# Kernel tuning notes

Hardware: AMD Instinct MI355X
Metric: run time of the kernel (lower is better)

## Reference

```python
import jax, jax.numpy as jnp
import numpy as np

DS = 8        # downsample_dim
PRUNE = 0.9


def _prune(w, rate):
    # DNW-style magnitude pruning: keep top (1-rate) fraction of |w|.
    thr = jnp.percentile(jnp.abs(w), rate * 100.0)
    mask = (jnp.abs(w) >= thr).astype(w.dtype)
    # straight-through: forward uses w*mask, backward passes dense grad to w
    return w - jax.lax.stop_gradient(w - w * mask)


def _conv2d(x, k):
    return jax.lax.conv_general_dilated(
        x, k, (1, 1), 'SAME', dimension_numbers=('NCHW', 'OIHW', 'NCHW'))


def _instance_norm(x, gamma, beta, eps=1e-5):
    mu = x.mean(axis=(2, 3), keepdims=True)
    var = ((x - mu) ** 2).mean(axis=(2, 3), keepdims=True)
    xn = (x - mu) * jax.lax.rsqrt(var + eps)
    return xn * gamma[None, :, None, None] + beta[None, :, None, None]


def _graph(x, w1, w2):
    B, C, H, W = x.shape
    f = H // DS
    # average-pool down to DS x DS, flatten channels*spatial into graph nodes
    pooled = x.reshape(B, C, DS, f, DS, f).mean(axis=(3, 5))  # [B, C, DS, DS]
    nodes = pooled.reshape(B, C * DS * DS)                    # [B, N]
    h = jax.nn.relu(nodes @ _prune(w1, PRUNE).T)              # [B, feature_dim]
    out = h @ _prune(w2, PRUNE).T                             # [B, N]
    out = out.reshape(B, C, DS, DS)
    # nearest-neighbor upsample back to H x W
    out = jnp.repeat(jnp.repeat(out, f, axis=2), f, axis=3)
    return out


def setup_inputs() -> dict:
    key = jax.random.key(0)
    ks = jax.random.split(key, 4)
    B, C, H, W = 32, 256, 32, 32
    N = C * DS * DS   # 16384 nodes
    FEAT = 2048       # feature_dim
    x = jax.random.normal(ks[0], (B, C, H, W), jnp.float32)
    conv_w = jax.random.normal(ks[1], (C, C, 3, 3), jnp.float32) / np.sqrt(C * 9)
    w1 = jax.random.normal(ks[2], (FEAT, N), jnp.float32) / np.sqrt(N)
    w2 = jax.random.normal(ks[3], (N, FEAT), jnp.float32) / np.sqrt(FEAT)
    gamma = jnp.ones((C,), jnp.float32)
    beta = jnp.zeros((C,), jnp.float32)
    return {"x": x, "conv_w": conv_w, "w1": w1, "w2": w2,
            "gamma": gamma, "beta": beta, "t": 0}


def reference(x, conv_w, w1, w2, gamma, beta, t):
    # t is the ODE time; unused by the forward math (as in the original module)
    out = jax.nn.relu(x)
    out = _conv2d(out, conv_w)
    out = _graph(out, w1, w2)
    out = _instance_norm(out, gamma, beta)
    return out
```

## Files before the change

kernel.cpp:

```cpp
#include <hip/hip_runtime.h>
#include <stdint.h>


typedef float f32x4 __attribute__((ext_vector_type(4)));
typedef __bf16 bf16x8 __attribute__((ext_vector_type(8)));

#define NBATCH 32
#define NCH    256
#define NNODE  16384
#define FEATD  2048
#define KCONV  2304

static constexpr long long NW    = 33554432LL;
static constexpr double    POS_D = 0.9 * (double)(NW - 1);
static constexpr int       K0    = (int)POS_D;

static constexpr int WAVE_CAP = 768;
static constexpr int NSEG     = 4096;
static constexpr int OVCAP    = 65536;
static constexpr int EBUF_CAP = 8192;

static constexpr size_t OFF_APOOL = 0;
static constexpr size_t OFF_NODES = 9437184;
static constexpr size_t OFF_HF32  = 10485760;
static constexpr size_t OFF_HB    = 10747904;
static constexpr size_t OFF_G     = 10878976;
static constexpr size_t OFF_SHIST = 12976128;
static constexpr size_t OFF_GHIST = 12992512;
static constexpr size_t OFF_CTRL  = 13025280;
static constexpr size_t OFF_EBUF  = 13025408;
static constexpr size_t OFF_CNT   = 13058176;
static constexpr size_t OFF_BLW   = 13074560;
static constexpr size_t OFF_CBUF  = 13090944;
static constexpr size_t OFF_OVF   = OFF_CBUF + (size_t)NSEG * WAVE_CAP * 4;
static constexpr size_t WS_MIN    = OFF_OVF + (size_t)OVCAP * 4;

struct Ctrl {
  unsigned vlo, vhi, shift, nov;
  unsigned e_lo, e_hi, base_e, nex;
  unsigned b0, b1, dbg, pad;
  float thr, a, b;
  unsigned pad2;
};

__device__ __forceinline__ float prune1(float v, float thr) {
  return fabsf(v) >= thr ? v : 0.0f;
}


__global__ void k_sample_hist(const float* __restrict__ w, unsigned* __restrict__ hist) {
  __shared__ unsigned lh[4096];
  int t = threadIdx.x;
  for (int i = t; i < 4096; i += 256) lh[i] = 0;
  __syncthreads();
  const float4* p = (const float4*)(w + (size_t)blockIdx.x * 65536);
  float4 v = p[t];
  {
    unsigned k;
    k = (__float_as_uint(v.x) & 0x7fffffffu) >> 19; atomicAdd(&lh[k], 1u);
    k = (__float_as_uint(v.y) & 0x7fffffffu) >> 19; atomicAdd(&lh[k], 1u);
    k = (__float_as_uint(v.z) & 0x7fffffffu) >> 19; atomicAdd(&lh[k], 1u);
    k = (__float_as_uint(v.w) & 0x7fffffffu) >> 19; atomicAdd(&lh[k], 1u);
  }
  __syncthreads();
  for (int i = t; i < 4096; i += 256)
    if (lh[i]) atomicAdd(&hist[i], lh[i]);
}

__global__ void k_range2(const unsigned* __restrict__ hist, Ctrl* __restrict__ c) {
  __shared__ unsigned csum[256];
  __shared__ unsigned pre[256];
  __shared__ unsigned res[2];
  int t = threadIdx.x;
  unsigned loc[16];
  unsigned s = 0;
  for (int i = 0; i < 16; ++i) { loc[i] = hist[t * 16 + i]; s += loc[i]; }
  csum[t] = s;
  __syncthreads();
  if (t == 0) {
    unsigned acc = 0;
    for (int i = 0; i < 256; ++i) { pre[i] = acc; acc += csum[i]; }
  }
  __syncthreads();
  const int m = 524288, qm = 471859, MR = 2000;
  int targ[2] = { qm - MR, qm + MR };
  for (int k = 0; k < 2; ++k) {
    int r = targ[k];
    if (r < 0) r = 0;
    if (r >= m) r = m - 1;
    if ((int)pre[t] <= r && r < (int)(pre[t] + csum[t])) {
      unsigned acc = pre[t];
      for (int i = 0; i < 16; ++i) {
        acc += loc[i];
        if ((int)acc > r) { res[k] = (unsigned)(t * 16 + i); break; }
      }
    }
  }
  __syncthreads();
  if (t == 0) {
    int lo = (int)res[0];
    int hi = (int)res[1];
    if (hi - lo + 1 > 8) hi = lo + 7;
    c->vlo = (unsigned)lo << 19;
    c->vhi = (unsigned)(hi + 1) << 19;
    unsigned span = c->vhi - c->vlo;
    unsigned sh = 0;
    while ((span >> sh) > 8192u) sh++;
    c->shift = sh;
    c->nov = 0; c->nex = 0;
    c->thr = 0.f;
  }
}

__global__ void k_compact(const float* __restrict__ w, unsigned* __restrict__ cbuf,
                          unsigned* __restrict__ ovf, unsigned* __restrict__ counts,
                          unsigned* __restrict__ belows, Ctrl* __restrict__ c) {
  __shared__ unsigned lbuf[4][WAVE_CAP];
  int t = threadIdx.x, wv = t >> 6, lane = t & 63;
  unsigned vlo = c->vlo, vhi = c->vhi;
  unsigned below = 0;
  unsigned cnt = 0;
  unsigned long long lanemask = (1ull << lane) - 1ull;
  const float4* p = (const float4*)(w + (size_t)blockIdx.x * 32768);
  for (int it = 0; it < 32; ++it) {
    float4 v = p[it * 256 + t];
    float comps[4] = { v.x, v.y, v.z, v.w };
#pragma unroll
    for (int j = 0; j < 4; ++j) {
      unsigned key = __float_as_uint(comps[j]) & 0x7fffffffu;
      below += (key < vlo) ? 1u : 0u;
      bool in = (key >= vlo) && (key < vhi);
      unsigned long long msk = __ballot(in);
      if (in) {
        unsigned slot = cnt + (unsigned)__popcll(msk & lanemask);
        if (slot < (unsigned)WAVE_CAP) lbuf[wv][slot] = key;
        else {
          unsigned ps = atomicAdd(&c->nov, 1u);
          if (ps < (unsigned)OVCAP) ovf[ps] = key;
        }
      }
      cnt += (unsigned)__popcll(msk);
    }
  }
  for (int off = 1; off < 64; off <<= 1) below += __shfl_xor(below, off);
  unsigned staged = cnt < (unsigned)WAVE_CAP ? cnt : (unsigned)WAVE_CAP;
  int s = blockIdx.x * 4 + wv;
  unsigned* dst = cbuf + (size_t)s * WAVE_CAP;
  for (unsigned i = lane; i < staged; i += 64) dst[i] = lbuf[wv][i];
  if (lane == 0) { counts[s] = staged; belows[s] = below; }
}

__global__ void k_sel_hist(const unsigned* __restrict__ cbuf, const unsigned* __restrict__ ovf,
                           const unsigned* __restrict__ counts, unsigned* __restrict__ gh,
                           const Ctrl* __restrict__ c) {
  __shared__ unsigned h[8192];
  int t = threadIdx.x;
  for (int i = t; i < 8192; i += 256) h[i] = 0;
  __syncthreads();
  unsigned vlo = c->vlo, sh = c->shift;
  for (int i = 0; i < 64; ++i) {
    int s = blockIdx.x * 64 + i;
    unsigned n = counts[s];
    const unsigned* seg = cbuf + (size_t)s * WAVE_CAP;
    for (unsigned k = t; k < n; k += 256)
      atomicAdd(&h[(seg[k] - vlo) >> sh], 1u);
  }
  if (blockIdx.x == 0) {
    unsigned nov = c->nov; if (nov > (unsigned)OVCAP) nov = OVCAP;
    for (unsigned k = t; k < nov; k += 256)
      atomicAdd(&h[(ovf[k] - vlo) >> sh], 1u);
  }
  __syncthreads();
  for (int i = t; i < 8192; i += 256)
    if (h[i]) atomicAdd(&gh[i], h[i]);
}

__global__ void k_sel_bin(const unsigned* __restrict__ gh, const unsigned* __restrict__ counts,
                          const unsigned* __restrict__ belows, Ctrl* __restrict__ c) {
  __shared__ unsigned rb[256], rc[256];
  __shared__ unsigned cs[256];
  __shared__ unsigned pre[257];
  __shared__ int bsel[2];
  __shared__ unsigned pbase[2];
  __shared__ long long tot_below, tot_nin;
  int t = threadIdx.x;
  unsigned bsum = 0, csum2 = 0;
  for (int i = 0; i < 16; ++i) { bsum += belows[t * 16 + i]; csum2 += counts[t * 16 + i]; }
  rb[t] = bsum; rc[t] = csum2;
  unsigned loc[32];
  unsigned s = 0;
  for (int i = 0; i < 32; ++i) { loc[i] = gh[t * 32 + i]; s += loc[i]; }
  cs[t] = s;
  __syncthreads();
  if (t == 0) {
    unsigned acc = 0;
    for (int i = 0; i < 256; ++i) { pre[i] = acc; acc += cs[i]; }
    pre[256] = acc;
    long long a = 0, b = 0;
    for (int i = 0; i < 256; ++i) { a += rb[i]; b += rc[i]; }
    unsigned nov = c->nov; if (nov > (unsigned)OVCAP) nov = OVCAP;
    tot_below = a; tot_nin = b + nov;
    bsel[0] = 0; bsel[1] = 0; pbase[0] = 0; pbase[1] = 0;
  }
  __syncthreads();
  long long nin = tot_nin;
  long long below = tot_below;
  for (int k = 0; k < 2; ++k) {
    long long r = (long long)(K0 + k) - below;
    if (r < 0) r = 0;
    if (r >= nin) r = nin - 1;
    if ((long long)pre[t] <= r && r < (long long)pre[t] + (long long)cs[t]) {
      unsigned acc = pre[t];
      for (int i = 0; i < 32; ++i) {
        if ((long long)(acc + loc[i]) > r) { bsel[k] = t * 32 + i; pbase[k] = acc; break; }
        acc += loc[i];
      }
    }
    __syncthreads();
  }
  if (t == 0) {
    int b0 = bsel[0], b1 = bsel[1];
    c->b0 = (unsigned)b0; c->b1 = (unsigned)b1;
    c->e_lo = c->vlo + ((unsigned)b0 << c->shift);
    c->e_hi = c->vlo + ((unsigned)(b1 + 1) << c->shift);
    c->base_e = (unsigned)(below + (long long)pbase[0]);
    c->nex = 0;
  }
}

__global__ void k_extract(const unsigned* __restrict__ cbuf, const unsigned* __restrict__ ovf,
                          const unsigned* __restrict__ counts, unsigned* __restrict__ ebuf,
                          Ctrl* __restrict__ c) {
  unsigned e_lo = c->e_lo, e_hi = c->e_hi;
  int t = threadIdx.x;
  for (int i = 0; i < 64; ++i) {
    int s = blockIdx.x * 64 + i;
    unsigned n = counts[s];
    const unsigned* seg = cbuf + (size_t)s * WAVE_CAP;
    for (unsigned k = t; k < n; k += 256) {
      unsigned key = seg[k];
      if (key >= e_lo && key < e_hi) {
        unsigned p = atomicAdd(&c->nex, 1u);
        if (p < (unsigned)EBUF_CAP) ebuf[p] = key;
      }
    }
  }
  if (blockIdx.x == 0) {
    unsigned nov = c->nov; if (nov > (unsigned)OVCAP) nov = OVCAP;
    for (unsigned k = t; k < nov; k += 256) {
      unsigned key = ovf[k];
      if (key >= e_lo && key < e_hi) {
        unsigned p = atomicAdd(&c->nex, 1u);
        if (p < (unsigned)EBUF_CAP) ebuf[p] = key;
      }
    }
  }
}

__global__ void k_final(const unsigned* __restrict__ ebuf, Ctrl* __restrict__ c,
                        double frac) {
  __shared__ unsigned keys[EBUF_CAP];
  __shared__ unsigned abits, bbits;
  int t = threadIdx.x;
  int n = (int)c->nex; if (n > EBUF_CAP) n = EBUF_CAP;
  for (int i = t; i < n; i += 256) keys[i] = ebuf[i];
  if (t == 0) { abits = 0; bbits = 0; }
  __syncthreads();
  long long r0 = (long long)K0 - (long long)c->base_e;
  long long r1 = r0 + 1;
  if (r0 < 0) r0 = 0; if (r0 > n - 1) r0 = n - 1;
  if (r1 < 0) r1 = 0; if (r1 > n - 1) r1 = n - 1;
  for (int i = t; i < n; i += 256) {
    unsigned k = keys[i];
    int cl = 0, ce = 0;
    for (int j = 0; j < n; ++j) {
      cl += (keys[j] < k) ? 1 : 0;
      ce += (keys[j] <= k) ? 1 : 0;
    }
    if ((long long)cl <= r0 && r0 < (long long)ce) abits = k;
    if ((long long)cl <= r1 && r1 < (long long)ce) bbits = k;
  }
  __syncthreads();
  if (t == 0) {
    double a = (double)__uint_as_float(abits);
    double b = (double)__uint_as_float(bbits);
    c->a = (float)a; c->b = (float)b;
    c->thr = (float)(a + frac * (b - a));
  }
}


__global__ void k_pool(const float* __restrict__ x, __bf16* __restrict__ apool) {
  __shared__ float lds[4][1024];
  __shared__ float V[4][24][32];
  int t = threadIdx.x, wv = t >> 6, lane = t & 63;
  int p = blockIdx.x * 4 + wv;
  int b = p >> 8, cch = p & 255;
  const float* xp = x + (size_t)p * 1024;
  for (int q = 0; q < 4; ++q) {
    float4 v = ((const float4*)xp)[q * 64 + lane];
    int idx = (q * 64 + lane) * 4;
    lds[wv][idx + 0] = fmaxf(v.x, 0.f);
    lds[wv][idx + 1] = fmaxf(v.y, 0.f);
    lds[wv][idx + 2] = fmaxf(v.z, 0.f);
    lds[wv][idx + 3] = fmaxf(v.w, 0.f);
  }
  __syncthreads();
  for (int e = lane; e < 768; e += 64) {
    int vi = e >> 5, ccol = e & 31;
    int i = vi / 3, dy = vi % 3;
    int r0 = 4 * i + dy - 1;
    float s = 0.f;
#pragma unroll
    for (int u = 0; u < 4; ++u) {
      int r = r0 + u;
      if (r >= 0 && r < 32) s += lds[wv][r * 32 + ccol];
    }
    V[wv][vi][ccol] = s;
  }
  __syncthreads();
  int pos = lane, i = pos >> 3, j = pos & 7;
  __bf16* ap = apool + (size_t)(b * 64 + pos) * KCONV + cch * 9;
#pragma unroll
  for (int dy = 0; dy < 3; ++dy) {
    int vi = i * 3 + dy;
#pragma unroll
    for (int dx = 0; dx < 3; ++dx) {
      int c0 = 4 * j + dx - 1;
      float s = 0.f;
#pragma unroll
      for (int v4 = 0; v4 < 4; ++v4) {
        int cc = c0 + v4;
        if (cc >= 0 && cc < 32) s += V[wv][vi][cc];
      }
      ap[dy * 3 + dx] = (__bf16)(s * 0.0625f);
    }
  }
}

__global__ void k_convgemm(const __bf16* __restrict__ apool, const float* __restrict__ cw,
                           __bf16* __restrict__ nodes) {
  int t = threadIdx.x, wv = t >> 6, l = t & 63;
  int cb = blockIdx.x & 15;
  int rg = blockIdx.x >> 4;
  int row0 = rg * 256 + wv * 64;
  int cbase = cb * 16;
  int kofs = (l >> 4) * 8;
  f32x4 acc[4] = {};
  const float* aw = cw + (size_t)(cbase + (l & 15)) * KCONV + kofs;
  for (int kk = 0; kk < KCONV; kk += 32) {
    float4 a0 = *(const float4*)(aw + kk);
    float4 a1 = *(const float4*)(aw + kk + 4);
    bf16x8 af;
    af[0] = (__bf16)a0.x; af[1] = (__bf16)a0.y; af[2] = (__bf16)a0.z; af[3] = (__bf16)a0.w;
    af[4] = (__bf16)a1.x; af[5] = (__bf16)a1.y; af[6] = (__bf16)a1.z; af[7] = (__bf16)a1.w;
#pragma unroll
    for (int rt = 0; rt < 4; ++rt) {
      const __bf16* bp = apool + (size_t)(row0 + rt * 16 + (l & 15)) * KCONV + kk + kofs;
      bf16x8 bv = *(const bf16x8*)bp;
      acc[rt] = __builtin_amdgcn_mfma_f32_16x16x32_bf16(af, bv, acc[rt], 0, 0, 0);
    }
  }
#pragma unroll
  for (int rt = 0; rt < 4; ++rt) {
    int prow = row0 + rt * 16 + (l & 15);
    int bidx = prow >> 6, pos = prow & 63;
#pragma unroll
    for (int j = 0; j < 4; ++j) {
      int cc = cbase + (l >> 4) * 4 + j;
      nodes[(size_t)bidx * NNODE + cc * 64 + pos] = (__bf16)acc[rt][j];
    }
  }
}

__global__ void k_gemm1(const float* __restrict__ w1, const __bf16* __restrict__ nodes,
                        const Ctrl* __restrict__ ctrl, float* __restrict__ hf) {
  int t = threadIdx.x, wv = t >> 6, l = t & 63;
  int fb = blockIdx.x >> 5;
  int ks = blockIdx.x & 31;
  float thr = ctrl->thr;
  int kofs = (l >> 4) * 8;
  int kk0 = ks * 512;
  const float*  awp = w1 + (size_t)(fb * 64 + wv * 16 + (l & 15)) * NNODE + kk0 + kofs;
  const __bf16* b0p = nodes + (size_t)(l & 15) * NNODE + kk0 + kofs;
  const __bf16* b1p = nodes + (size_t)((l & 15) + 16) * NNODE + kk0 + kofs;
  f32x4 acc0 = {}, acc1 = {};
#pragma unroll 4
  for (int kk = 0; kk < 512; kk += 32) {
    float4 a0 = *(const float4*)(awp + kk);
    float4 a1 = *(const float4*)(awp + kk + 4);
    bf16x8 af;
    af[0] = (__bf16)prune1(a0.x, thr); af[1] = (__bf16)prune1(a0.y, thr);
    af[2] = (__bf16)prune1(a0.z, thr); af[3] = (__bf16)prune1(a0.w, thr);
    af[4] = (__bf16)prune1(a1.x, thr); af[5] = (__bf16)prune1(a1.y, thr);
    af[6] = (__bf16)prune1(a1.z, thr); af[7] = (__bf16)prune1(a1.w, thr);
    bf16x8 bv0 = *(const bf16x8*)(b0p + kk);
    bf16x8 bv1 = *(const bf16x8*)(b1p + kk);
    acc0 = __builtin_amdgcn_mfma_f32_16x16x32_bf16(af, bv0, acc0, 0, 0, 0);
    acc1 = __builtin_amdgcn_mfma_f32_16x16x32_bf16(af, bv1, acc1, 0, 0, 0);
  }
#pragma unroll
  for (int j = 0; j < 4; ++j) {
    int f = fb * 64 + wv * 16 + (l >> 4) * 4 + j;
    atomicAdd(&hf[f * 32 + (l & 15)], acc0[j]);
    atomicAdd(&hf[f * 32 + 16 + (l & 15)], acc1[j]);
  }
}

__global__ void k_relucvt(const float* __restrict__ hf, __bf16* __restrict__ hb) {
  int idx = blockIdx.x * 256 + threadIdx.x;
  float v = fmaxf(hf[idx], 0.f);
  int f = idx >> 5, b = idx & 31;
  hb[b * FEATD + f] = (__bf16)v;
}

__global__ void k_gemm2(const float* __restrict__ w2, const __bf16* __restrict__ hb,
                        const Ctrl* __restrict__ ctrl, float* __restrict__ g) {
  int t = threadIdx.x, wv = t >> 6, l = t & 63;
  int nb = blockIdx.x >> 2;
  int ks = blockIdx.x & 3;
  float thr = ctrl->thr;
  int kofs = (l >> 4) * 8;
  int kk0 = ks * 512;
  const float*  awp = w2 + (size_t)(nb * 64 + wv * 16 + (l & 15)) * FEATD + kk0 + kofs;
  const __bf16* b0p = hb + (size_t)(l & 15) * FEATD + kk0 + kofs;
  const __bf16* b1p = hb + (size_t)((l & 15) + 16) * FEATD + kk0 + kofs;
  f32x4 acc0 = {}, acc1 = {};
#pragma unroll 4
  for (int kk = 0; kk < 512; kk += 32) {
    float4 a0 = *(const float4*)(awp + kk);
    float4 a1 = *(const float4*)(awp + kk + 4);
    bf16x8 af;
    af[0] = (__bf16)prune1(a0.x, thr); af[1] = (__bf16)prune1(a0.y, thr);
    af[2] = (__bf16)prune1(a0.z, thr); af[3] = (__bf16)prune1(a0.w, thr);
    af[4] = (__bf16)prune1(a1.x, thr); af[5] = (__bf16)prune1(a1.y, thr);
    af[6] = (__bf16)prune1(a1.z, thr); af[7] = (__bf16)prune1(a1.w, thr);
    bf16x8 bv0 = *(const bf16x8*)(b0p + kk);
    bf16x8 bv1 = *(const bf16x8*)(b1p + kk);
    acc0 = __builtin_amdgcn_mfma_f32_16x16x32_bf16(af, bv0, acc0, 0, 0, 0);
    acc1 = __builtin_amdgcn_mfma_f32_16x16x32_bf16(af, bv1, acc1, 0, 0, 0);
  }
#pragma unroll
  for (int j = 0; j < 4; ++j) {
    int n = nb * 64 + wv * 16 + (l >> 4) * 4 + j;
    atomicAdd(&g[n * 32 + (l & 15)], acc0[j]);
    atomicAdd(&g[n * 32 + 16 + (l & 15)], acc1[j]);
  }
}

__global__ void k_normup(const float* __restrict__ g, const float* __restrict__ gamma,
                         const float* __restrict__ beta, float* __restrict__ out) {
  int t = threadIdx.x, wv = t >> 6, lane = t & 63;
  int id = blockIdx.x * 4 + wv;
  int b = id >> 8, cch = id & 255;
  float v = g[(size_t)(cch * 64 + lane) * 32 + b];
  float s = v;
  for (int off = 1; off < 64; off <<= 1) s += __shfl_xor(s, off);
  float mean = s * (1.0f / 64.0f);
  float d = v - mean;
  float q = d * d;
  for (int off = 1; off < 64; off <<= 1) q += __shfl_xor(q, off);
  float var = q * (1.0f / 64.0f);
  float y = d * rsqrtf(var + 1e-5f) * gamma[cch] + beta[cch];
  int i = lane >> 3, j = lane & 7;
  float4 y4 = { y, y, y, y };
  float* op = out + ((size_t)(b * 256 + cch) * 32 + i * 4) * 32 + j * 4;
#pragma unroll
  for (int u = 0; u < 4; ++u) *(float4*)(op + u * 32) = y4;
}


extern "C" void kernel_launch(void* const* d_in, const int* in_sizes, int n_in,
                              void* d_out, int out_size, void* d_ws, size_t ws_size,
                              hipStream_t stream) {
  const float* x      = (const float*)d_in[0];
  const float* conv_w = (const float*)d_in[1];
  const float* w1     = (const float*)d_in[2];
  const float* w2     = (const float*)d_in[3];
  const float* gamma  = (const float*)d_in[4];
  const float* beta   = (const float*)d_in[5];
  float* out = (float*)d_out;

  if (ws_size < WS_MIN) return;

  char* wsb = (char*)d_ws;
  __bf16*   apool  = (__bf16*)(wsb + OFF_APOOL);
  __bf16*   nodes  = (__bf16*)(wsb + OFF_NODES);
  float*    hf     = (float*)(wsb + OFF_HF32);
  __bf16*   hb     = (__bf16*)(wsb + OFF_HB);
  float*    g      = (float*)(wsb + OFF_G);
  unsigned* shist  = (unsigned*)(wsb + OFF_SHIST);
  unsigned* ghist  = (unsigned*)(wsb + OFF_GHIST);
  Ctrl*     ctrl   = (Ctrl*)(wsb + OFF_CTRL);
  unsigned* ebuf   = (unsigned*)(wsb + OFF_EBUF);
  unsigned* counts = (unsigned*)(wsb + OFF_CNT);
  unsigned* belows = (unsigned*)(wsb + OFF_BLW);
  unsigned* cbuf   = (unsigned*)(wsb + OFF_CBUF);
  unsigned* ovf    = (unsigned*)(wsb + OFF_OVF);

  const double frac = POS_D - (double)K0;
  const float* wm[2] = { w1, w2 };
  for (int m = 0; m < 2; ++m) {
    Ctrl* c = ctrl + m;
    hipMemsetAsync(shist, 0, 4096 * 4, stream);
    hipMemsetAsync(ghist, 0, 8192 * 4, stream);
    k_sample_hist<<<512, 256, 0, stream>>>(wm[m], shist);
    k_range2<<<1, 256, 0, stream>>>(shist, c);
    k_compact<<<1024, 256, 0, stream>>>(wm[m], cbuf, ovf, counts, belows, c);
    k_sel_hist<<<64, 256, 0, stream>>>(cbuf, ovf, counts, ghist, c);
    k_sel_bin<<<1, 256, 0, stream>>>(ghist, counts, belows, c);
    k_extract<<<64, 256, 0, stream>>>(cbuf, ovf, counts, ebuf, c);
    k_final<<<1, 256, 0, stream>>>(ebuf, c, frac);
  }

  k_pool<<<2048, 256, 0, stream>>>(x, apool);
  k_convgemm<<<128, 256, 0, stream>>>(apool, conv_w, nodes);

  hipMemsetAsync(hf, 0, 2048 * 32 * 4, stream);
  k_gemm1<<<1024, 256, 0, stream>>>(w1, nodes, ctrl + 0, hf);
  k_relucvt<<<256, 256, 0, stream>>>(hf, hb);

  hipMemsetAsync(g, 0, 16384 * 32 * 4, stream);
  k_gemm2<<<1024, 256, 0, stream>>>(w2, hb, ctrl + 1, g);

  k_normup<<<2048, 256, 0, stream>>>(g, gamma, beta, out);
}
```

Measured before the change: 636.3 us.

## Batch both weight-threshold pipelines into single launches and replace atomic split-K with partial buffers

The percentile-selection kernels for w1 and w2 now run together, using a second grid dimension or block index, with separate per-matrix buffers. This halves the number of launches and memsets and lets the two matrices fill the GPU at the same time. The split-K GEMMs now write their partial sums to separate buffers instead of doing float atomicAdd, and the consumer kernels (relu-convert, norm) add up the slices. This removes atomic contention and the memsets in exchange for more workspace and extra reads of the partial buffers.

```diff
diff --git a/kernel.cpp b/kernel.cpp
--- a/kernel.cpp
+++ b/kernel.cpp
@@ -22,18 +22,18 @@
 
 static constexpr size_t OFF_APOOL = 0;
 static constexpr size_t OFF_NODES = 9437184;
-static constexpr size_t OFF_HF32  = 10485760;
-static constexpr size_t OFF_HB    = 10747904;
-static constexpr size_t OFF_G     = 10878976;
-static constexpr size_t OFF_SHIST = 12976128;
-static constexpr size_t OFF_GHIST = 12992512;
-static constexpr size_t OFF_CTRL  = 13025280;
-static constexpr size_t OFF_EBUF  = 13025408;
-static constexpr size_t OFF_CNT   = 13058176;
-static constexpr size_t OFF_BLW   = 13074560;
-static constexpr size_t OFF_CBUF  = 13090944;
-static constexpr size_t OFF_OVF   = OFF_CBUF + (size_t)NSEG * WAVE_CAP * 4;
-static constexpr size_t WS_MIN    = OFF_OVF + (size_t)OVCAP * 4;
+static constexpr size_t OFF_HFP   = 10485760;
+static constexpr size_t OFF_HB    = 18874368;
+static constexpr size_t OFF_GP    = 19005440;
+static constexpr size_t OFF_SHIST = 27394048;
+static constexpr size_t OFF_GHIST = 27426816;
+static constexpr size_t OFF_CTRL  = 27492352;
+static constexpr size_t OFF_EBUF  = 27492480;
+static constexpr size_t OFF_CNT   = 27558016;
+static constexpr size_t OFF_BLW   = 27590784;
+static constexpr size_t OFF_CBUF  = 27623552;
+static constexpr size_t OFF_OVF   = 52789376;
+static constexpr size_t WS_MIN    = 53313664;
 
 struct Ctrl {
   unsigned vlo, vhi, shift, nov;
@@ -48,9 +48,12 @@
 }
 
 
-__global__ void k_sample_hist(const float* __restrict__ w, unsigned* __restrict__ hist) {
+__global__ void k_sample_hist(const float* __restrict__ w1, const float* __restrict__ w2,
+                              unsigned* __restrict__ hist) {
   __shared__ unsigned lh[4096];
-  int t = threadIdx.x;
+  int t = threadIdx.x, m = blockIdx.y;
+  const float* w = m ? w2 : w1;
+  unsigned* gh = hist + m * 4096;
   for (int i = t; i < 4096; i += 256) lh[i] = 0;
   __syncthreads();
   const float4* p = (const float4*)(w + (size_t)blockIdx.x * 65536);
@@ -64,17 +67,19 @@
   }
   __syncthreads();
   for (int i = t; i < 4096; i += 256)
-    if (lh[i]) atomicAdd(&hist[i], lh[i]);
-}
-
-__global__ void k_range2(const unsigned* __restrict__ hist, Ctrl* __restrict__ c) {
+    if (lh[i]) atomicAdd(&gh[i], lh[i]);
+}
+
+__global__ void k_range2(const unsigned* __restrict__ hist, Ctrl* __restrict__ ctrl) {
   __shared__ unsigned csum[256];
   __shared__ unsigned pre[256];
   __shared__ unsigned res[2];
-  int t = threadIdx.x;
+  int t = threadIdx.x, m = blockIdx.x;
+  const unsigned* gh = hist + m * 4096;
+  Ctrl* c = ctrl + m;
   unsigned loc[16];
   unsigned s = 0;
-  for (int i = 0; i < 16; ++i) { loc[i] = hist[t * 16 + i]; s += loc[i]; }
+  for (int i = 0; i < 16; ++i) { loc[i] = gh[t * 16 + i]; s += loc[i]; }
   csum[t] = s;
   __syncthreads();
   if (t == 0) {
@@ -82,12 +87,12 @@
     for (int i = 0; i < 256; ++i) { pre[i] = acc; acc += csum[i]; }
   }
   __syncthreads();
-  const int m = 524288, qm = 471859, MR = 2000;
+  const int msz = 524288, qm = 471859, MR = 2000;
   int targ[2] = { qm - MR, qm + MR };
   for (int k = 0; k < 2; ++k) {
     int r = targ[k];
     if (r < 0) r = 0;
-    if (r >= m) r = m - 1;
+    if (r >= msz) r = msz - 1;
     if ((int)pre[t] <= r && r < (int)(pre[t] + csum[t])) {
       unsigned acc = pre[t];
       for (int i = 0; i < 16; ++i) {
@@ -112,11 +117,19 @@
   }
 }
 
-__global__ void k_compact(const float* __restrict__ w, unsigned* __restrict__ cbuf,
-                          unsigned* __restrict__ ovf, unsigned* __restrict__ counts,
-                          unsigned* __restrict__ belows, Ctrl* __restrict__ c) {
+__global__ void k_compact(const float* __restrict__ w1, const float* __restrict__ w2,
+                          unsigned* __restrict__ cbuf_all, unsigned* __restrict__ ovf_all,
+                          unsigned* __restrict__ counts_all, unsigned* __restrict__ belows_all,
+                          Ctrl* __restrict__ ctrl) {
   __shared__ unsigned lbuf[4][WAVE_CAP];
   int t = threadIdx.x, wv = t >> 6, lane = t & 63;
+  int m = blockIdx.y;
+  const float* w = m ? w2 : w1;
+  unsigned* cbuf = cbuf_all + (size_t)m * NSEG * WAVE_CAP;
+  unsigned* ovf = ovf_all + (size_t)m * OVCAP;
+  unsigned* counts = counts_all + m * NSEG;
+  unsigned* belows = belows_all + m * NSEG;
+  Ctrl* c = ctrl + m;
   unsigned vlo = c->vlo, vhi = c->vhi;
   unsigned below = 0;
   unsigned cnt = 0;
@@ -150,11 +163,16 @@
   if (lane == 0) { counts[s] = staged; belows[s] = below; }
 }
 
-__global__ void k_sel_hist(const unsigned* __restrict__ cbuf, const unsigned* __restrict__ ovf,
-                           const unsigned* __restrict__ counts, unsigned* __restrict__ gh,
-                           const Ctrl* __restrict__ c) {
+__global__ void k_sel_hist(const unsigned* __restrict__ cbuf_all, const unsigned* __restrict__ ovf_all,
+                           const unsigned* __restrict__ counts_all, unsigned* __restrict__ gh_all,
+                           const Ctrl* __restrict__ ctrl) {
   __shared__ unsigned h[8192];
-  int t = threadIdx.x;
+  int t = threadIdx.x, m = blockIdx.y;
+  const unsigned* cbuf = cbuf_all + (size_t)m * NSEG * WAVE_CAP;
+  const unsigned* ovf = ovf_all + (size_t)m * OVCAP;
+  const unsigned* counts = counts_all + m * NSEG;
+  unsigned* gh = gh_all + m * 8192;
+  const Ctrl* c = ctrl + m;
   for (int i = t; i < 8192; i += 256) h[i] = 0;
   __syncthreads();
   unsigned vlo = c->vlo, sh = c->shift;
@@ -175,15 +193,19 @@
     if (h[i]) atomicAdd(&gh[i], h[i]);
 }
 
-__global__ void k_sel_bin(const unsigned* __restrict__ gh, const unsigned* __restrict__ counts,
-                          const unsigned* __restrict__ belows, Ctrl* __restrict__ c) {
+__global__ void k_sel_bin(const unsigned* __restrict__ gh_all, const unsigned* __restrict__ counts_all,
+                          const unsigned* __restrict__ belows_all, Ctrl* __restrict__ ctrl) {
   __shared__ unsigned rb[256], rc[256];
   __shared__ unsigned cs[256];
   __shared__ unsigned pre[257];
   __shared__ int bsel[2];
   __shared__ unsigned pbase[2];
   __shared__ long long tot_below, tot_nin;
-  int t = threadIdx.x;
+  int t = threadIdx.x, m = blockIdx.x;
+  const unsigned* gh = gh_all + m * 8192;
+  const unsigned* counts = counts_all + m * NSEG;
+  const unsigned* belows = belows_all + m * NSEG;
+  Ctrl* c = ctrl + m;
   unsigned bsum = 0, csum2 = 0;
   for (int i = 0; i < 16; ++i) { bsum += belows[t * 16 + i]; csum2 += counts[t * 16 + i]; }
   rb[t] = bsum; rc[t] = csum2;
@@ -228,11 +250,16 @@
   }
 }
 
-__global__ void k_extract(const unsigned* __restrict__ cbuf, const unsigned* __restrict__ ovf,
-                          const unsigned* __restrict__ counts, unsigned* __restrict__ ebuf,
-                          Ctrl* __restrict__ c) {
+__global__ void k_extract(const unsigned* __restrict__ cbuf_all, const unsigned* __restrict__ ovf_all,
+                          const unsigned* __restrict__ counts_all, unsigned* __restrict__ ebuf_all,
+                          Ctrl* __restrict__ ctrl) {
+  int t = threadIdx.x, m = blockIdx.y;
+  const unsigned* cbuf = cbuf_all + (size_t)m * NSEG * WAVE_CAP;
+  const unsigned* ovf = ovf_all + (size_t)m * OVCAP;
+  const unsigned* counts = counts_all + m * NSEG;
+  unsigned* ebuf = ebuf_all + m * EBUF_CAP;
+  Ctrl* c = ctrl + m;
   unsigned e_lo = c->e_lo, e_hi = c->e_hi;
-  int t = threadIdx.x;
   for (int i = 0; i < 64; ++i) {
     int s = blockIdx.x * 64 + i;
     unsigned n = counts[s];
@@ -257,11 +284,13 @@
   }
 }
 
-__global__ void k_final(const unsigned* __restrict__ ebuf, Ctrl* __restrict__ c,
+__global__ void k_final(const unsigned* __restrict__ ebuf_all, Ctrl* __restrict__ ctrl,
                         double frac) {
   __shared__ unsigned keys[EBUF_CAP];
   __shared__ unsigned abits, bbits;
-  int t = threadIdx.x;
+  int t = threadIdx.x, m = blockIdx.x;
+  const unsigned* ebuf = ebuf_all + m * EBUF_CAP;
+  Ctrl* c = ctrl + m;
   int n = (int)c->nex; if (n > EBUF_CAP) n = EBUF_CAP;
   for (int i = t; i < n; i += 256) keys[i] = ebuf[i];
   if (t == 0) { abits = 0; bbits = 0; }
@@ -374,7 +403,7 @@
 }
 
 __global__ void k_gemm1(const float* __restrict__ w1, const __bf16* __restrict__ nodes,
-                        const Ctrl* __restrict__ ctrl, float* __restrict__ hf) {
+                        const Ctrl* __restrict__ ctrl, float* __restrict__ hfp) {
   int t = threadIdx.x, wv = t >> 6, l = t & 63;
   int fb = blockIdx.x >> 5;
   int ks = blockIdx.x & 31;
@@ -399,23 +428,27 @@
     acc0 = __builtin_amdgcn_mfma_f32_16x16x32_bf16(af, bv0, acc0, 0, 0, 0);
     acc1 = __builtin_amdgcn_mfma_f32_16x16x32_bf16(af, bv1, acc1, 0, 0, 0);
   }
+  float* dst = hfp + (size_t)ks * 65536;
 #pragma unroll
   for (int j = 0; j < 4; ++j) {
     int f = fb * 64 + wv * 16 + (l >> 4) * 4 + j;
-    atomicAdd(&hf[f * 32 + (l & 15)], acc0[j]);
-    atomicAdd(&hf[f * 32 + 16 + (l & 15)], acc1[j]);
-  }
-}
-
-__global__ void k_relucvt(const float* __restrict__ hf, __bf16* __restrict__ hb) {
+    dst[f * 32 + (l & 15)] = acc0[j];
+    dst[f * 32 + 16 + (l & 15)] = acc1[j];
+  }
+}
+
+__global__ void k_relucvt(const float* __restrict__ hfp, __bf16* __restrict__ hb) {
   int idx = blockIdx.x * 256 + threadIdx.x;
-  float v = fmaxf(hf[idx], 0.f);
+  float s = 0.f;
+#pragma unroll
+  for (int ks = 0; ks < 32; ++ks) s += hfp[(size_t)ks * 65536 + idx];
+  float v = fmaxf(s, 0.f);
   int f = idx >> 5, b = idx & 31;
   hb[b * FEATD + f] = (__bf16)v;
 }
 
 __global__ void k_gemm2(const float* __restrict__ w2, const __bf16* __restrict__ hb,
-                        const Ctrl* __restrict__ ctrl, float* __restrict__ g) {
+                        const Ctrl* __restrict__ ctrl, float* __restrict__ gp) {
   int t = threadIdx.x, wv = t >> 6, l = t & 63;
   int nb = blockIdx.x >> 2;
   int ks = blockIdx.x & 3;
@@ -440,20 +473,22 @@
     acc0 = __builtin_amdgcn_mfma_f32_16x16x32_bf16(af, bv0, acc0, 0, 0, 0);
     acc1 = __builtin_amdgcn_mfma_f32_16x16x32_bf16(af, bv1, acc1, 0, 0, 0);
   }
+  float* dst = gp + (size_t)ks * 524288;
 #pragma unroll
   for (int j = 0; j < 4; ++j) {
     int n = nb * 64 + wv * 16 + (l >> 4) * 4 + j;
-    atomicAdd(&g[n * 32 + (l & 15)], acc0[j]);
-    atomicAdd(&g[n * 32 + 16 + (l & 15)], acc1[j]);
-  }
-}
-
-__global__ void k_normup(const float* __restrict__ g, const float* __restrict__ gamma,
+    dst[n * 32 + (l & 15)] = acc0[j];
+    dst[n * 32 + 16 + (l & 15)] = acc1[j];
+  }
+}
+
+__global__ void k_normup(const float* __restrict__ gp, const float* __restrict__ gamma,
                          const float* __restrict__ beta, float* __restrict__ out) {
   int t = threadIdx.x, wv = t >> 6, lane = t & 63;
   int id = blockIdx.x * 4 + wv;
   int b = id >> 8, cch = id & 255;
-  float v = g[(size_t)(cch * 64 + lane) * 32 + b];
+  size_t gi = (size_t)(cch * 64 + lane) * 32 + b;
+  float v = gp[gi] + gp[gi + 524288] + gp[gi + 2 * 524288] + gp[gi + 3 * 524288];
   float s = v;
   for (int off = 1; off < 64; off <<= 1) s += __shfl_xor(s, off);
   float mean = s * (1.0f / 64.0f);
@@ -486,9 +521,9 @@
   char* wsb = (char*)d_ws;
   __bf16*   apool  = (__bf16*)(wsb + OFF_APOOL);
   __bf16*   nodes  = (__bf16*)(wsb + OFF_NODES);
-  float*    hf     = (float*)(wsb + OFF_HF32);
+  float*    hfp    = (float*)(wsb + OFF_HFP);
   __bf16*   hb     = (__bf16*)(wsb + OFF_HB);
-  float*    g      = (float*)(wsb + OFF_G);
+  float*    gp     = (float*)(wsb + OFF_GP);
   unsigned* shist  = (unsigned*)(wsb + OFF_SHIST);
   unsigned* ghist  = (unsigned*)(wsb + OFF_GHIST);
   Ctrl*     ctrl   = (Ctrl*)(wsb + OFF_CTRL);
@@ -499,29 +534,24 @@
   unsigned* ovf    = (unsigned*)(wsb + OFF_OVF);
 
   const double frac = POS_D - (double)K0;
-  const float* wm[2] = { w1, w2 };
-  for (int m = 0; m < 2; ++m) {
-    Ctrl* c = ctrl + m;
-    hipMemsetAsync(shist, 0, 4096 * 4, stream);
-    hipMemsetAsync(ghist, 0, 8192 * 4, stream);
-    k_sample_hist<<<512, 256, 0, stream>>>(wm[m], shist);
-    k_range2<<<1, 256, 0, stream>>>(shist, c);
-    k_compact<<<1024, 256, 0, stream>>>(wm[m], cbuf, ovf, counts, belows, c);
-    k_sel_hist<<<64, 256, 0, stream>>>(cbuf, ovf, counts, ghist, c);
-    k_sel_bin<<<1, 256, 0, stream>>>(ghist, counts, belows, c);
-    k_extract<<<64, 256, 0, stream>>>(cbuf, ovf, counts, ebuf, c);
-    k_final<<<1, 256, 0, stream>>>(ebuf, c, frac);
-  }
+
+  hipMemsetAsync(shist, 0, (OFF_CTRL - OFF_SHIST), stream);
+
+  k_sample_hist<<<dim3(512, 2), 256, 0, stream>>>(w1, w2, shist);
+  k_range2<<<2, 256, 0, stream>>>(shist, ctrl);
+  k_compact<<<dim3(1024, 2), 256, 0, stream>>>(w1, w2, cbuf, ovf, counts, belows, ctrl);
+  k_sel_hist<<<dim3(64, 2), 256, 0, stream>>>(cbuf, ovf, counts, ghist, ctrl);
+  k_sel_bin<<<2, 256, 0, stream>>>(ghist, counts, belows, ctrl);
+  k_extract<<<dim3(64, 2), 256, 0, stream>>>(cbuf, ovf, counts, ebuf, ctrl);
+  k_final<<<2, 256, 0, stream>>>(ebuf, ctrl, frac);
 
   k_pool<<<2048, 256, 0, stream>>>(x, apool);
   k_convgemm<<<128, 256, 0, stream>>>(apool, conv_w, nodes);
 
-  hipMemsetAsync(hf, 0, 2048 * 32 * 4, stream);
-  k_gemm1<<<1024, 256, 0, stream>>>(w1, nodes, ctrl + 0, hf);
-  k_relucvt<<<256, 256, 0, stream>>>(hf, hb);
-
-  hipMemsetAsync(g, 0, 16384 * 32 * 4, stream);
-  k_gemm2<<<1024, 256, 0, stream>>>(w2, hb, ctrl + 1, g);
-
-  k_normup<<<2048, 256, 0, stream>>>(g, gamma, beta, out);
-}
+  k_gemm1<<<1024, 256, 0, stream>>>(w1, nodes, ctrl + 0, hfp);
+  k_relucvt<<<256, 256, 0, stream>>>(hfp, hb);
+
+  k_gemm2<<<1024, 256, 0, stream>>>(w2, hb, ctrl + 1, gp);
+
+  k_normup<<<2048, 256, 0, stream>>>(gp, gamma, beta, out);
+}
```

Result: faster. 554.2 us (-12.9%).
